# Optimization experiments

Measured on AMD Instinct MI355X. Metric: run time of the kernel, lower is better.

The kernel has to match this reference:

```python
import jax, jax.numpy as jnp
import numpy as np

DIM = 384
HEADS = 12
K = 3          # kernel_size
PAD = 1
STRIDE = 1
B, H, W = 8, 56, 56


def conv1x1(x, w, b=None):
    # x: [B,C,H,W], w: [O,C]
    y = jnp.einsum('bchw,oc->bohw', x, w)
    if b is not None:
        y = y + b[None, :, None, None]
    return y


def unfold(x, k, p, s):
    # torch nn.Unfold: returns patches [B, C, k*k, nH, nW], kernel row-major, channel-major overall
    Bx, C, Hx, Wx = x.shape
    nH = (Hx + 2 * p - k) // s + 1
    nW = (Wx + 2 * p - k) // s + 1
    xp = jnp.pad(x, ((0, 0), (0, 0), (p, p), (p, p)))
    cols = [xp[:, :, i:i + s * nH:s, j:j + s * nW:s] for i in range(k) for j in range(k)]
    return jnp.stack(cols, axis=2), nH, nW


def fold(col, Hx, Wx, k, p, s):
    # torch F.fold (col2im): scatter-add overlapping windows. col: [B, C, k*k, nH, nW]
    Bx, C, _, nH, nW = col.shape
    canvas = jnp.zeros((Bx, C, Hx + 2 * p, Wx + 2 * p), col.dtype)
    idx = 0
    for i in range(k):
        for j in range(k):
            canvas = canvas.at[:, :, i:i + s * nH:s, j:j + s * nW:s].add(col[:, :, idx])
            idx += 1
    return canvas[:, :, p:p + Hx, p:p + Wx]


def setup_inputs() -> dict:
    key = jax.random.key(0)
    ks = jax.random.split(key, 5)
    k2 = K * K
    x = jax.random.normal(ks[0], (B, DIM, H, W), dtype=jnp.float32)
    v_w = jax.random.normal(ks[1], (DIM, DIM), dtype=jnp.float32) * 0.02
    v_b = jnp.zeros((DIM,), dtype=jnp.float32)
    attn_w = jax.random.normal(ks[2], (k2 * k2 * HEADS, DIM), dtype=jnp.float32) * 0.02
    proj_w = jax.random.normal(ks[3], (DIM, DIM), dtype=jnp.float32) * 0.02
    return {'x': x, 'v_w': v_w, 'v_b': v_b, 'attn_w': attn_w, 'proj_w': proj_w}


def reference(x, v_w, v_b, attn_w, proj_w):
    Bx, C, Hx, Wx = x.shape
    k2 = K * K
    hd = C // HEADS  # head dim
    # value projection + unfold into overlapping k x k windows
    v = conv1x1(x, v_w, v_b)
    vcol, nH, nW = unfold(v, K, PAD, STRIDE)        # [B, C, k2, nH, nW]
    L = nH * nW
    v = vcol.reshape(Bx, HEADS, hd, k2, L)          # split C = (heads, hd), heads slow
    v = v.transpose(0, 1, 4, 3, 2)                  # [B, n, L, k2(d), hd]
    # adaptive avg pool to (nH, nW); with stride=1 this is identity (pool window 1)
    ph, pw = Hx // nH, Wx // nW
    xp = x.reshape(Bx, C, nH, ph, nW, pw).mean(axis=(3, 5))
    # per-pixel attention logits, channel layout = ((i*k2 + d)*HEADS + head)
    a = jnp.einsum('bchw,oc->bohw', xp, attn_w)     # [B, k2*k2*n, nH, nW]
    a = a.reshape(Bx, k2, k2, HEADS, L)             # [B, i, d, n, L]
    a = a.transpose(0, 3, 4, 1, 2)                  # [B, n, L, i, d]
    a = jax.nn.softmax(a, axis=-1)
    out = jnp.einsum('bnlid,bnldh->bnlih', a, v)    # [B, n, L, i, hd]
    out = out.transpose(0, 1, 4, 3, 2)              # [B, n, hd, i, L] -> channel (n*hd+h)
    out = out.reshape(Bx, C, k2, nH, nW)
    out = fold(out, Hx, Wx, K, PAD, STRIDE)         # scatter-add windows back
    return conv1x1(out, proj_w)
```

## Files before the change

### kernel.cpp

```cpp
#include <hip/hip_runtime.h>
#include <hip/hip_bf16.h>

#define DIM   384
#define HEADS 12
#define K2    9
#define HH    56
#define WW    56
#define HWP   3136
#define BB    8
#define AO    972
#define AOP   1024
#define MCAT  1408
#define PP    3200

typedef __hip_bfloat16 bf16;
typedef short bf16x8 __attribute__((ext_vector_type(8)));
typedef short bf16x4v __attribute__((ext_vector_type(4)));
typedef float f32x4 __attribute__((ext_vector_type(4)));

static __device__ __forceinline__ float b2f(bf16 v) { return __bfloat162float(v); }
static __device__ __forceinline__ float bs2f(short s) {
    return __uint_as_float(((unsigned int)(unsigned short)s) << 16);
}
static __device__ __forceinline__ short f2bs(float f) {
    __hip_bfloat16 h = __float2bfloat16(f);
    return *(short*)&h;
}

static __device__ __forceinline__ void gl_lds16(const bf16* g, bf16* l) {
    __builtin_amdgcn_global_load_lds(
        (const __attribute__((address_space(1))) unsigned int*)g,
        (__attribute__((address_space(3))) unsigned int*)l, 16, 0, 0);
}

__global__ __launch_bounds__(256) void prep_kernel(
        const float* __restrict__ x, const float* __restrict__ v_w,
        const float* __restrict__ attn_w, const float* __restrict__ proj_w,
        bf16* __restrict__ xT, bf16* __restrict__ wcat, bf16* __restrict__ wp) {
    const int bid = blockIdx.x;
    if (bid < 400) {
        const int lane = threadIdx.x & 63, w = threadIdx.x >> 6;
        const int p = (bid % 50) * 64 + lane;
        const int b = bid / 50;
        bf16* dst = xT + ((size_t)b * PP + p) * DIM;
        if (p >= HWP) {
            bf16x8 z = {};
            for (int cg = w; cg < 48; cg += 4) *(bf16x8*)(dst + cg * 8) = z;
            return;
        }
        const float* src = x + (size_t)b * DIM * HWP + p;
        for (int cg = w; cg < 48; cg += 4) {
            bf16x8 v;
#pragma unroll
            for (int j = 0; j < 8; j++) v[j] = f2bs(src[(size_t)(cg * 8 + j) * HWP]);
            *(bf16x8*)(dst + cg * 8) = v;
        }
    } else {
        const int idx = (bid - 400) * 256 + threadIdx.x;
        const int NCAT = MCAT * DIM;
        if (idx < NCAT) {
            const int row = idx / DIM, col = idx % DIM;
            float v;
            if (row < 384) v = v_w[row * DIM + col];
            else { const int r2 = row - 384; v = (r2 < AO) ? attn_w[r2 * DIM + col] : 0.f; }
            *(short*)&wcat[idx] = f2bs(v);
        } else {
            const int j = idx - NCAT;
            if (j < 384 * DIM) *(short*)&wp[j] = f2bs(proj_w[j]);
        }
    }
}

#define GEMM_MAIN_LOOP_V4(Ab, Bb, lA, lB, acc)                                 \
    for (int k0 = 0; k0 < DIM; k0 += 64) {                                     \
        _Pragma("unroll")                                                      \
        for (int r = 0; r < 4; r++) {                                          \
            int idx = r * 256 + t;                                             \
            int row = idx >> 3;                                                \
            int kq = ((idx & 7) - (row >> 1)) & 7;                             \
            gl_lds16(Ab + (size_t)row * DIM + k0 + kq * 8, lA + idx * 8);      \
        }                                                                      \
        _Pragma("unroll")                                                      \
        for (int r = 0; r < 4; r++) {                                          \
            int idx = r * 256 + t;                                             \
            int row = idx >> 3;                                                \
            int kq = ((idx & 7) - (row >> 1)) & 7;                             \
            gl_lds16(Bb + (size_t)row * DIM + k0 + kq * 8, lB + idx * 8);      \
        }                                                                      \
        __syncthreads();                                                       \
        _Pragma("unroll")                                                      \
        for (int h = 0; h < 2; h++) {                                          \
            const int swzh = (((h << 2) + quad + (l16 >> 1)) & 7) * 8;         \
            bf16x8 af[4], bfr[4];                                              \
            _Pragma("unroll")                                                  \
            for (int mt = 0; mt < 4; mt++)                                     \
                af[mt] = *(const bf16x8*)(lA + (wm * 64 + mt * 16 + l16) * 64 + swzh); \
            _Pragma("unroll")                                                  \
            for (int nt = 0; nt < 4; nt++)                                     \
                bfr[nt] = *(const bf16x8*)(lB + (wn * 64 + nt * 16 + l16) * 64 + swzh); \
            _Pragma("unroll")                                                  \
            for (int mt = 0; mt < 4; mt++)                                     \
                _Pragma("unroll")                                              \
                for (int nt = 0; nt < 4; nt++)                                 \
                    acc[mt][nt] = __builtin_amdgcn_mfma_f32_16x16x32_bf16(     \
                        af[mt], bfr[nt], acc[mt][nt], 0, 0, 0);                \
        }                                                                      \
        __syncthreads();                                                       \
    }

__global__ __launch_bounds__(256) void gemm12_kernel(
        const bf16* __restrict__ A, const bf16* __restrict__ Bt,
        const float* __restrict__ bias, bf16* __restrict__ vT,
        bf16* __restrict__ lT) {
    __shared__ bf16 lds[16384];
    bf16* lA = lds;
    bf16* lB = lds + 8192;
    const int t = threadIdx.x;
    const int lane = t & 63, w = t >> 6;
    const int wm = w & 1, wn = w >> 1;
    const int quad = lane >> 4, l16 = lane & 15;
    const int n0 = blockIdx.x * 128;
    const int m0 = blockIdx.y * 128;
    const int b = blockIdx.z;

    const bf16* Ab = A + (size_t)m0 * DIM;
    const bf16* Bb = Bt + ((size_t)b * PP + n0) * DIM;

    f32x4 acc[4][4] = {};
    GEMM_MAIN_LOOP_V4(Ab, Bb, lA, lB, acc)

    const bool isv = (m0 < 384);
    bf16* outp = isv ? vT : lT;
    const int ostr = isv ? DIM : AOP;
    const int ch0 = isv ? m0 : m0 - 384;

    bf16* wbuf = lds + w * 1152;
    const int nr = lane >> 2;
    const int mc = (lane & 3) * 16;
#pragma unroll
    for (int nt = 0; nt < 4; nt++) {
#pragma unroll
        for (int mt = 0; mt < 4; mt++) {
            float4 bi = make_float4(0.f, 0.f, 0.f, 0.f);
            if (isv) bi = *(const float4*)(bias + ch0 + wm * 64 + mt * 16 + quad * 4);
            bf16x4v pk;
            pk[0] = f2bs(acc[mt][nt][0] + bi.x);
            pk[1] = f2bs(acc[mt][nt][1] + bi.y);
            pk[2] = f2bs(acc[mt][nt][2] + bi.z);
            pk[3] = f2bs(acc[mt][nt][3] + bi.w);
            *(bf16x4v*)(wbuf + l16 * 72 + mt * 16 + quad * 4) = pk;
        }
        bf16x8 v0 = *(const bf16x8*)(wbuf + nr * 72 + mc);
        bf16x8 v1 = *(const bf16x8*)(wbuf + nr * 72 + mc + 8);
        const int p = n0 + wn * 64 + nt * 16 + nr;
        if (p < HWP) {
            bf16* dp = outp + ((size_t)b * PP + p) * ostr + ch0 + wm * 64 + mc;
            *(bf16x8*)dp = v0;
            *(bf16x8*)(dp + 8) = v1;
        }
    }
}

__global__ __launch_bounds__(256) void gemm_planar_kernel(
        const bf16* __restrict__ A, const bf16* __restrict__ Bt,
        float* __restrict__ out) {
    __shared__ bf16 lds[16384];
    bf16* lA = lds;
    bf16* lB = lds + 8192;
    const int t = threadIdx.x;
    const int lane = t & 63, w = t >> 6;
    const int wm = w & 1, wn = w >> 1;
    const int quad = lane >> 4, l16 = lane & 15;
    const int n0 = blockIdx.x * 128;
    const int m0 = blockIdx.y * 128;
    const int b = blockIdx.z;

    const bf16* Ab = A + (size_t)m0 * DIM;
    const bf16* Bb = Bt + ((size_t)b * PP + n0) * DIM;

    f32x4 acc[4][4] = {};
    GEMM_MAIN_LOOP_V4(Ab, Bb, lA, lB, acc)

#pragma unroll
    for (int mt = 0; mt < 4; mt++) {
#pragma unroll
        for (int nt = 0; nt < 4; nt++) {
            int p = n0 + wn * 64 + nt * 16 + l16;
            if (p >= HWP) continue;
#pragma unroll
            for (int reg = 0; reg < 4; reg++) {
                int o = m0 + wm * 64 + mt * 16 + quad * 4 + reg;
                out[((size_t)b * DIM + o) * HWP + p] = acc[mt][nt][reg];
            }
        }
    }
}

__global__ __launch_bounds__(384) void attn_fold_kernel(
        const bf16* __restrict__ lT, const bf16* __restrict__ vT,
        bf16* __restrict__ cT) {
    __shared__ bf16 P[8 * 9 * 12 * 9];
    __shared__ float Wf[8 * 25 * 12];
    const int t = threadIdx.x;
    const int b = blockIdx.y;
    const int pix0 = blockIdx.x * 8;
    const int Y = pix0 / WW, X0 = pix0 % WW;

    for (int r = t; r < 864; r += 384) {
        const int px = r / 108, rem = r % 108;
        const int i = rem / 12, n = rem % 12;
        const int ir = i / 3, ic = i % 3;
        const int yi = Y + 1 - ir, xi = X0 + px + 1 - ic;
        bf16* Pd = &P[r * 9];
        if (yi < 0 || yi >= HH || xi < 0 || xi >= WW) {
#pragma unroll
            for (int d = 0; d < K2; d++) *(short*)&Pd[d] = 0;
        } else {
            const bf16* base = lT + ((size_t)b * PP + yi * WW + xi) * AOP + i * 108 + n;
            float lv[K2];
            float m = -1e30f;
#pragma unroll
            for (int d = 0; d < K2; d++) {
                lv[d] = b2f(base[d * 12]);
                m = fmaxf(m, lv[d]);
            }
            float s = 0.f;
#pragma unroll
            for (int d = 0; d < K2; d++) { lv[d] = __expf(lv[d] - m); s += lv[d]; }
            const float inv = 1.f / s;
#pragma unroll
            for (int d = 0; d < K2; d++) *(short*)&Pd[d] = f2bs(lv[d] * inv);
        }
    }
    __syncthreads();

    for (int e = t; e < 2400; e += 384) {
        const int px = e / 300, rem = e % 300;
        const int off = rem / 12, n = rem % 12;
        const int dy = off / 5 - 2, dx = off % 5 - 2;
        const int ir_lo = max(0, -dy), ir_hi = min(2, 2 - dy);
        const int ic_lo = max(0, -dx), ic_hi = min(2, 2 - dx);
        float wsum = 0.f;
        for (int ir = ir_lo; ir <= ir_hi; ir++)
            for (int ic = ic_lo; ic <= ic_hi; ic++) {
                const int i = ir * 3 + ic;
                const int d = (dy + ir) * 3 + (dx + ic);
                wsum += b2f(P[((px * 9 + i) * 12 + n) * 9 + d]);
            }
        Wf[e] = wsum;
    }
    __syncthreads();

    const int px = t / 48, cg = t % 48;
    const int X = X0 + px;
    const int n = cg >> 2;
    const float* Wp = &Wf[px * 300];
    const bf16* vb = vT + (size_t)b * PP * DIM;
    float acc[8] = {};
#pragma unroll
    for (int dy = -2; dy <= 2; dy++) {
        const int ny = Y + dy;
        if (ny < 0 || ny >= HH) continue;
#pragma unroll
        for (int dx = -2; dx <= 2; dx++) {
            const int nx = X + dx;
            const bool ok = (nx >= 0 && nx < WW);
            const int nxc = min(max(nx, 0), WW - 1);
            const float w = ok ? Wp[((dy + 2) * 5 + dx + 2) * 12 + n] : 0.f;
            bf16x8 vv = *(const bf16x8*)(vb + (size_t)(ny * WW + nxc) * DIM + cg * 8);
#pragma unroll
            for (int j = 0; j < 8; j++) acc[j] += w * bs2f(vv[j]);
        }
    }
    bf16x8 po;
#pragma unroll
    for (int j = 0; j < 8; j++) po[j] = f2bs(acc[j]);
    *(bf16x8*)(cT + ((size_t)b * PP + pix0 + px) * DIM + cg * 8) = po;
}

extern "C" void kernel_launch(void* const* d_in, const int* in_sizes, int n_in,
                              void* d_out, int out_size, void* d_ws, size_t ws_size,
                              hipStream_t stream) {
    const float* x      = (const float*)d_in[0];
    const float* v_w    = (const float*)d_in[1];
    const float* v_b    = (const float*)d_in[2];
    const float* attn_w = (const float*)d_in[3];
    const float* proj_w = (const float*)d_in[4];
    float* out = (float*)d_out;

    bf16* xT    = (bf16*)d_ws;
    bf16* vT    = xT + (size_t)BB * PP * DIM;
    bf16* lT    = vT + (size_t)BB * PP * DIM;
    bf16* wcat  = lT + (size_t)BB * PP * AOP;
    bf16* wp    = wcat + (size_t)MCAT * DIM;
    bf16* cT    = xT;

    const int NW = MCAT * DIM + 384 * DIM;
    const int nprep = 400 + (NW + 255) / 256;
    prep_kernel<<<nprep, 256, 0, stream>>>(x, v_w, attn_w, proj_w, xT, wcat, wp);

    gemm12_kernel<<<dim3(PP / 128, MCAT / 128, BB), 256, 0, stream>>>(wcat, xT, v_b, vT, lT);
    attn_fold_kernel<<<dim3(HWP / 8, BB), 384, 0, stream>>>(lT, vT, cT);
    gemm_planar_kernel<<<dim3(PP / 128, 3, BB), 256, 0, stream>>>(wp, cT, out);
}
```

Before: 220.0 us.

## Permute attention weight rows so softmax logits are contiguous per head

Reorders the attention-logit rows of the concatenated weight matrix to an (i, head, d padded to 10) layout. Each softmax group of 9 logits then sits contiguously in memory and is read with five 32-bit loads instead of nine strided 16-bit loads. The price is padding the logit channels from 1024 to 1152, so the fused GEMM does more work (MCAT grows from 1408 to 1536) and writes a larger intermediate.

Result: no change. 221.8 us (+0.8%).

```diff
diff --git a/kernel.cpp b/kernel.cpp
--- a/kernel.cpp
+++ b/kernel.cpp
@@ -9,8 +9,8 @@
 #define HWP   3136
 #define BB    8
 #define AO    972
-#define AOP   1024
-#define MCAT  1408
+#define AOP2  1152
+#define MCAT  1536
 #define PP    3200
 
 typedef __hip_bfloat16 bf16;
@@ -21,6 +21,12 @@
 static __device__ __forceinline__ float b2f(bf16 v) { return __bfloat162float(v); }
 static __device__ __forceinline__ float bs2f(short s) {
     return __uint_as_float(((unsigned int)(unsigned short)s) << 16);
+}
+static __device__ __forceinline__ float lou(unsigned int u) {
+    return __uint_as_float(u << 16);
+}
+static __device__ __forceinline__ float hiu(unsigned int u) {
+    return __uint_as_float(u & 0xffff0000u);
 }
 static __device__ __forceinline__ short f2bs(float f) {
     __hip_bfloat16 h = __float2bfloat16(f);
@@ -60,9 +66,17 @@
         const int NCAT = MCAT * DIM;
         if (idx < NCAT) {
             const int row = idx / DIM, col = idx % DIM;
-            float v;
-            if (row < 384) v = v_w[row * DIM + col];
-            else { const int r2 = row - 384; v = (r2 < AO) ? attn_w[r2 * DIM + col] : 0.f; }
+            float v = 0.f;
+            if (row < 384) {
+                v = v_w[row * DIM + col];
+            } else {
+                const int q = row - 384;
+                if (q < 1080) {
+                    const int i = q / 120, rem = q % 120;
+                    const int n = rem / 10, d = rem % 10;
+                    if (d < 9) v = attn_w[((i * 9 + d) * 12 + n) * DIM + col];
+                }
+            }
             *(short*)&wcat[idx] = f2bs(v);
         } else {
             const int j = idx - NCAT;
@@ -131,7 +145,7 @@
 
     const bool isv = (m0 < 384);
     bf16* outp = isv ? vT : lT;
-    const int ostr = isv ? DIM : AOP;
+    const int ostr = isv ? DIM : AOP2;
     const int ch0 = isv ? m0 : m0 - 384;
 
     bf16* wbuf = lds + w * 1152;
@@ -216,14 +230,20 @@
 #pragma unroll
             for (int d = 0; d < K2; d++) *(short*)&Pd[d] = 0;
         } else {
-            const bf16* base = lT + ((size_t)b * PP + yi * WW + xi) * AOP + i * 108 + n;
+            const bf16* rowp = lT + ((size_t)b * PP + yi * WW + xi) * AOP2
+                               + i * 120 + n * 10;
+            const unsigned int* up = (const unsigned int*)rowp;
+            const unsigned int u0 = up[0], u1 = up[1], u2 = up[2],
+                               u3 = up[3], u4 = up[4];
             float lv[K2];
+            lv[0] = lou(u0); lv[1] = hiu(u0);
+            lv[2] = lou(u1); lv[3] = hiu(u1);
+            lv[4] = lou(u2); lv[5] = hiu(u2);
+            lv[6] = lou(u3); lv[7] = hiu(u3);
+            lv[8] = lou(u4);
             float m = -1e30f;
 #pragma unroll
-            for (int d = 0; d < K2; d++) {
-                lv[d] = b2f(base[d * 12]);
-                m = fmaxf(m, lv[d]);
-            }
+            for (int d = 0; d < K2; d++) m = fmaxf(m, lv[d]);
             float s = 0.f;
 #pragma unroll
             for (int d = 0; d < K2; d++) { lv[d] = __expf(lv[d] - m); s += lv[d]; }
@@ -291,7 +311,7 @@
     bf16* xT    = (bf16*)d_ws;
     bf16* vT    = xT + (size_t)BB * PP * DIM;
     bf16* lT    = vT + (size_t)BB * PP * DIM;
-    bf16* wcat  = lT + (size_t)BB * PP * AOP;
+    bf16* wcat  = lT + (size_t)BB * PP * AOP2;
     bf16* wp    = wcat + (size_t)MCAT * DIM;
     bf16* cT    = xT;
 
```

## Permute attention logit channels for contiguous softmax loads and XCD-aware GEMM tile mapping

Applied to the files above, without the earlier changes.

The prep kernel permutes attn_w rows so the nine softmax logits per (pixel, window offset, head) sit next to each other in lT. The attention kernel can then read them with six 32-bit loads instead of nine strided bf16 loads. Both GEMM kernels switch to a flat 1D grid remapped so that blocks sharing the same B tile (batch and pixel tile) land on the same XCD for L2 reuse. The risk is an index mistake in the permutation or in the remap; with 2200 and 600 blocks the grid still covers every tile exactly once.

Result: no change. 223.8 us (+1.7%).

```diff
diff --git a/kernel.cpp b/kernel.cpp
--- a/kernel.cpp
+++ b/kernel.cpp
@@ -21,6 +21,12 @@
 static __device__ __forceinline__ float b2f(bf16 v) { return __bfloat162float(v); }
 static __device__ __forceinline__ float bs2f(short s) {
     return __uint_as_float(((unsigned int)(unsigned short)s) << 16);
+}
+static __device__ __forceinline__ float lou(unsigned int u) {
+    return __uint_as_float(u << 16);
+}
+static __device__ __forceinline__ float hiu(unsigned int u) {
+    return __uint_as_float(u & 0xffff0000u);
 }
 static __device__ __forceinline__ short f2bs(float f) {
     __hip_bfloat16 h = __float2bfloat16(f);
@@ -60,9 +66,17 @@
         const int NCAT = MCAT * DIM;
         if (idx < NCAT) {
             const int row = idx / DIM, col = idx % DIM;
-            float v;
-            if (row < 384) v = v_w[row * DIM + col];
-            else { const int r2 = row - 384; v = (r2 < AO) ? attn_w[r2 * DIM + col] : 0.f; }
+            float v = 0.f;
+            if (row < 384) {
+                v = v_w[row * DIM + col];
+            } else {
+                const int q = row - 384;
+                if (q < AO) {
+                    const int i = q / 108, rem = q % 108;
+                    const int n = rem / 9, d = rem % 9;
+                    v = attn_w[((i * 9 + d) * 12 + n) * DIM + col];
+                }
+            }
             *(short*)&wcat[idx] = f2bs(v);
         } else {
             const int j = idx - NCAT;
@@ -119,9 +133,14 @@
     const int lane = t & 63, w = t >> 6;
     const int wm = w & 1, wn = w >> 1;
     const int quad = lane >> 4, l16 = lane & 15;
-    const int n0 = blockIdx.x * 128;
-    const int m0 = blockIdx.y * 128;
-    const int b = blockIdx.z;
+
+    const int bid = blockIdx.x;
+    const int xcd = bid & 7, slot = bid >> 3;
+    const int m = slot % 11, gg = slot / 11;
+    const int g = xcd + 8 * gg;
+    const int n = g % 25, b = g / 25;
+    const int n0 = n * 128;
+    const int m0 = m * 128;
 
     const bf16* Ab = A + (size_t)m0 * DIM;
     const bf16* Bb = Bt + ((size_t)b * PP + n0) * DIM;
@@ -171,9 +190,14 @@
     const int lane = t & 63, w = t >> 6;
     const int wm = w & 1, wn = w >> 1;
     const int quad = lane >> 4, l16 = lane & 15;
-    const int n0 = blockIdx.x * 128;
-    const int m0 = blockIdx.y * 128;
-    const int b = blockIdx.z;
+
+    const int bid = blockIdx.x;
+    const int xcd = bid & 7, slot = bid >> 3;
+    const int m = slot % 3, gg = slot / 3;
+    const int g = xcd + 8 * gg;
+    const int n = g % 25, b = g / 25;
+    const int n0 = n * 128;
+    const int m0 = m * 128;
 
     const bf16* Ab = A + (size_t)m0 * DIM;
     const bf16* Bb = Bt + ((size_t)b * PP + n0) * DIM;
@@ -216,14 +240,23 @@
 #pragma unroll
             for (int d = 0; d < K2; d++) *(short*)&Pd[d] = 0;
         } else {
-            const bf16* base = lT + ((size_t)b * PP + yi * WW + xi) * AOP + i * 108 + n;
+            const bf16* rowp = lT + ((size_t)b * PP + yi * WW + xi) * AOP;
+            const int e0 = i * 108 + n * 9;
+            const unsigned int* up = (const unsigned int*)(rowp + (e0 & ~1));
+            float el[12];
+#pragma unroll
+            for (int j = 0; j < 6; j++) {
+                const unsigned int u = up[j];
+                el[2 * j] = lou(u);
+                el[2 * j + 1] = hiu(u);
+            }
+            const bool odd = (e0 & 1);
             float lv[K2];
+#pragma unroll
+            for (int d = 0; d < K2; d++) lv[d] = odd ? el[d + 1] : el[d];
             float m = -1e30f;
 #pragma unroll
-            for (int d = 0; d < K2; d++) {
-                lv[d] = b2f(base[d * 12]);
-                m = fmaxf(m, lv[d]);
-            }
+            for (int d = 0; d < K2; d++) m = fmaxf(m, lv[d]);
             float s = 0.f;
 #pragma unroll
             for (int d = 0; d < K2; d++) { lv[d] = __expf(lv[d] - m); s += lv[d]; }
@@ -299,7 +332,7 @@
     const int nprep = 400 + (NW + 255) / 256;
     prep_kernel<<<nprep, 256, 0, stream>>>(x, v_w, attn_w, proj_w, xT, wcat, wp);
 
-    gemm12_kernel<<<dim3(PP / 128, MCAT / 128, BB), 256, 0, stream>>>(wcat, xT, v_b, vT, lT);
+    gemm12_kernel<<<8 * 11 * 25, 256, 0, stream>>>(wcat, xT, v_b, vT, lT);
     attn_fold_kernel<<<dim3(HWP / 8, BB), 384, 0, stream>>>(lT, vT, cT);
-    gemm_planar_kernel<<<dim3(PP / 128, 3, BB), 256, 0, stream>>>(wp, cT, out);
-}
+    gemm_planar_kernel<<<8 * 3 * 25, 256, 0, stream>>>(wp, cT, out);
+}
```
